# Kernel optimization log

Measured on AMD Instinct MI355X. Metric: run time of the kernel, lower is better.

Reference implementation:

```python
import jax, jax.numpy as jnp
import numpy as np

C, S, H = 64, 2048, 512
ITERATIONS = 3

def squash(x, eps=1e-07):
    # per-vector squash along last dim: (|x|^2/(1+|x|^2)) * x/|x|
    sq = jnp.sum(x * x, axis=-1, keepdims=True)
    safe_norm = jnp.sqrt(sq + eps)
    scale = sq / (1.0 + sq)
    return scale * (x / safe_norm)

def setup_inputs() -> dict:
    key = jax.random.key(0)
    k1, k2 = jax.random.split(key)
    x = jax.random.normal(k1, (C * S, H), dtype=jnp.float32)
    # xavier-normal init for Linear(H, H)
    std = np.sqrt(2.0 / (H + H)).astype(np.float32)
    W_weight = jax.random.normal(k2, (H, H), dtype=jnp.float32) * std
    W_bias = jnp.zeros((H,), dtype=jnp.float32)
    return {"x": x, "W_weight": W_weight, "W_bias": W_bias}

def reference(x, W_weight, W_bias):
    xr = x.reshape(C, S, H)
    # e_ij = squash(Linear(x))  -> [C, S, H]
    e_ij = squash(jnp.einsum('csh,oh->cso', xr, W_weight) + W_bias)
    b_ij = jnp.zeros((C, S), dtype=x.dtype)
    c_i = jnp.zeros((C, H), dtype=x.dtype)
    for _ in range(ITERATIONS):
        d_i = jax.nn.softmax(b_ij, axis=1)[..., None]          # [C, S, 1]
        c_i = squash(jnp.sum(d_i * e_ij, axis=1))              # [C, H]
        b_ij = b_ij + jnp.einsum('csh,ch->cs', e_ij, c_i)      # [C, S]
    return c_i
```

## Files before the change

### kernel.cpp

```cpp
#include <hip/hip_runtime.h>
#include <hip/hip_fp16.h>

#define HDIM 512

typedef __fp16 fp16x2 __attribute__((ext_vector_type(2)));
typedef _Float16 h8 __attribute__((ext_vector_type(8)));
typedef __attribute__((ext_vector_type(4))) float floatx4;

__device__ __forceinline__ void lds_barrier() {
  asm volatile("s_waitcnt lgkmcnt(0)\n\ts_barrier" ::: "memory");
}
__device__ __forceinline__ void issue_fence() {
  asm volatile("" ::: "memory");
}

__global__ __launch_bounds__(256) void prep_w_kernel(
    const float* __restrict__ W, _Float16* __restrict__ wf) {
  int i = (blockIdx.x * 256 + threadIdx.x) * 4;
  float4 f = *(const float4*)(W + i);
  wf[i + 0] = (_Float16)f.x;
  wf[i + 1] = (_Float16)f.y;
  wf[i + 2] = (_Float16)f.z;
  wf[i + 3] = (_Float16)f.w;
}

#define XS_H (128 * 40)
#define WS_H (512 * 32)

__device__ __forceinline__ void issue_w_dma(const _Float16* __restrict__ wf,
                                            _Float16* dst, int kt, int tid,
                                            int widx) {
#pragma unroll
  for (int q = 0; q < 4; ++q) {
    int idx = q * 512 + tid;
    int n = idx >> 2;
    int src = (idx & 3) ^ ((n >> 1) & 3);
    size_t goff = (size_t)n * HDIM + kt * 32 + src * 8;
    __builtin_amdgcn_global_load_lds(
        (const __attribute__((address_space(1))) void*)(wf + goff),
        (__attribute__((address_space(3))) void*)(dst +
                                                  (q * 512 + widx * 64) * 8),
        16, 0, 0);
  }
}

__global__ __launch_bounds__(512, 2) void gemm_kernel(
    const float* __restrict__ x, const _Float16* __restrict__ wf,
    const float* __restrict__ bias, __half* __restrict__ e,
    float* __restrict__ u_part, float* __restrict__ den_part) {
  __shared__ __align__(16) _Float16 smem[2 * XS_H + 3 * WS_H];
  _Float16* xs[2] = {smem, smem + XS_H};
  _Float16* wsm = smem + 2 * XS_H;

  const int tid = threadIdx.x;
  const int lane = tid & 63;
  const int widx = tid >> 6;
  const int wave_m = widx >> 2;
  const int wave_n = widx & 3;
  const int lrow = lane & 15, quad = lane >> 4;

  const int bid = blockIdx.x;
  const int row0 = bid * 128;

  const int xrow = tid >> 2;
  const int xcg = tid & 3;
  const float* xbase = x + (size_t)(row0 + xrow) * HDIM + xcg * 8;

  floatx4 acc[4][8];
#pragma unroll
  for (int i = 0; i < 4; ++i)
#pragma unroll
    for (int j = 0; j < 8; ++j) acc[i][j] = (floatx4){0.f, 0.f, 0.f, 0.f};

  float4 xr[2][2];

  issue_w_dma(wf, wsm + 0 * WS_H, 0, tid, widx);
  issue_fence();
  xr[0][0] = *(const float4*)xbase;
  xr[0][1] = *(const float4*)(xbase + 4);
  issue_fence();
  issue_w_dma(wf, wsm + 1 * WS_H, 1, tid, widx);
  issue_fence();
  xr[1][0] = *(const float4*)(xbase + 32);
  xr[1][1] = *(const float4*)(xbase + 36);
  issue_fence();

  const int chunkB = quad ^ ((lrow >> 1) & 3);

#pragma unroll
  for (int t = 0; t < 16; ++t) {
    {
      float4 a0 = xr[t & 1][0], a1 = xr[t & 1][1];
      union { h8 v8; fp16x2 v2[4]; } u;
      u.v2[0] = __builtin_amdgcn_cvt_pkrtz(a0.x, a0.y);
      u.v2[1] = __builtin_amdgcn_cvt_pkrtz(a0.z, a0.w);
      u.v2[2] = __builtin_amdgcn_cvt_pkrtz(a1.x, a1.y);
      u.v2[3] = __builtin_amdgcn_cvt_pkrtz(a1.z, a1.w);
      *(h8*)&xs[t & 1][xrow * 40 + xcg * 8] = u.v8;
    }
    lds_barrier();
    if (t <= 13) {
      issue_w_dma(wf, wsm + ((t + 2) % 3) * WS_H, t + 2, tid, widx);
      issue_fence();
      const float* gp = xbase + (t + 2) * 32;
      xr[t & 1][0] = *(const float4*)gp;
      xr[t & 1][1] = *(const float4*)(gp + 4);
      issue_fence();
    }
    const _Float16* xsr = xs[t & 1];
    const _Float16* wcur = wsm + (t % 3) * WS_H;
    h8 a[4], bh[8];
#pragma unroll
    for (int mt = 0; mt < 4; ++mt)
      a[mt] = *(const h8*)&xsr[(wave_m * 64 + mt * 16 + lrow) * 40 + quad * 8];
#pragma unroll
    for (int nt = 0; nt < 8; ++nt)
      bh[nt] =
          *(const h8*)&wcur[(wave_n * 128 + nt * 16 + lrow) * 32 + chunkB * 8];
    __builtin_amdgcn_s_setprio(1);
#pragma unroll
    for (int mt = 0; mt < 4; ++mt)
#pragma unroll
      for (int nt = 0; nt < 8; ++nt)
        acc[mt][nt] = __builtin_amdgcn_mfma_f32_16x16x32_f16(
            a[mt], bh[nt], acc[mt][nt], 0, 0, 0);
    __builtin_amdgcn_s_setprio(0);
  }

  float* sqp = (float*)smem;
  float* scs = (float*)smem + 512;
  float* upl = (float*)smem + 640;

  float bias_v[8];
  int colg[8];
#pragma unroll
  for (int nt = 0; nt < 8; ++nt) {
    colg[nt] = wave_n * 128 + nt * 16 + lrow;
    bias_v[nt] = bias[colg[nt]];
  }
#pragma unroll
  for (int mt = 0; mt < 4; ++mt) {
#pragma unroll
    for (int r = 0; r < 4; ++r) {
      float s = 0.f;
#pragma unroll
      for (int nt = 0; nt < 8; ++nt) {
        float yv = acc[mt][nt][r] + bias_v[nt];
        s += yv * yv;
      }
      s += __shfl_xor(s, 1, 64);
      s += __shfl_xor(s, 2, 64);
      s += __shfl_xor(s, 4, 64);
      s += __shfl_xor(s, 8, 64);
      if (lrow == 0)
        sqp[wave_n * 128 + wave_m * 64 + mt * 16 + quad * 4 + r] = s;
    }
  }
  lds_barrier();
  if (tid < 128) {
    float s = sqp[tid] + sqp[128 + tid] + sqp[256 + tid] + sqp[384 + tid];
    scs[tid] = s / ((1.f + s) * sqrtf(s + 1e-7f));
  }
  lds_barrier();

  float up[8] = {0.f, 0.f, 0.f, 0.f, 0.f, 0.f, 0.f, 0.f};
#pragma unroll
  for (int mt = 0; mt < 4; ++mt) {
#pragma unroll
    for (int r = 0; r < 4; ++r) {
      int row_local = wave_m * 64 + mt * 16 + quad * 4 + r;
      float scv = scs[row_local];
      __half* erow = e + (size_t)(row0 + row_local) * HDIM;
#pragma unroll
      for (int nt = 0; nt < 8; ++nt) {
        float ev = (acc[mt][nt][r] + bias_v[nt]) * scv;
        erow[colg[nt]] = __float2half(ev);
        up[nt] += ev;
      }
    }
  }
#pragma unroll
  for (int nt = 0; nt < 8; ++nt) {
    float v = up[nt];
    v += __shfl_xor(v, 16, 64);
    v += __shfl_xor(v, 32, 64);
    if (quad == 0) upl[wave_m * 512 + colg[nt]] = v;
  }
  lds_barrier();
  u_part[(size_t)bid * HDIM + tid] = upl[tid] + upl[512 + tid];
  if (tid == 0) den_part[bid] = 128.0f;
}

__global__ __launch_bounds__(256) void kbv_kernel(
    const __half* __restrict__ e, float* __restrict__ b,
    const float* __restrict__ c_buf, float* __restrict__ u_part,
    float* __restrict__ den_part) {
  const int w = threadIdx.x >> 6;
  const int lane = threadIdx.x & 63;
  const int wave_g = blockIdx.x * 4 + w;
  const int cap = wave_g >> 6;
  const int chunk = wave_g & 63;
  const int r0 = cap * 2048 + chunk * 32;

  float c8[8];
  {
    const float4* cp = (const float4*)(c_buf + cap * HDIM + lane * 8);
    float4 ca = cp[0], cb = cp[1];
    c8[0] = ca.x; c8[1] = ca.y; c8[2] = ca.z; c8[3] = ca.w;
    c8[4] = cb.x; c8[5] = cb.y; c8[6] = cb.z; c8[7] = cb.w;
  }
  float u8[8] = {0, 0, 0, 0, 0, 0, 0, 0};
  float den = 0.f;

  union U { int4 v; __half hh[8]; };
  U cur[4], nxt[4];
  const __half* yb = e + (size_t)r0 * HDIM + lane * 8;
#pragma unroll
  for (int j = 0; j < 4; ++j) cur[j].v = *(const int4*)(yb + (size_t)j * HDIM);

  for (int g = 0; g < 8; ++g) {
    const int rg = r0 + g * 4;
    if (g < 7) {
#pragma unroll
      for (int j = 0; j < 4; ++j)
        nxt[j].v = *(const int4*)(yb + (size_t)(g * 4 + 4 + j) * HDIM);
    }
    float bv[4];
#pragma unroll
    for (int j = 0; j < 4; ++j) bv[j] = b[rg + j];
    float dot[4];
#pragma unroll
    for (int j = 0; j < 4; ++j) {
      float d = 0.f;
#pragma unroll
      for (int k = 0; k < 8; ++k) d += __half2float(cur[j].hh[k]) * c8[k];
      dot[j] = d;
    }
#pragma unroll
    for (int s = 1; s < 64; s <<= 1) {
#pragma unroll
      for (int j = 0; j < 4; ++j) dot[j] += __shfl_xor(dot[j], s, 64);
    }
#pragma unroll
    for (int j = 0; j < 4; ++j) {
      float bn = bv[j] + dot[j];
      if (lane == 0) b[rg + j] = bn;
      float wj = __expf(bn);
      den += wj;
#pragma unroll
      for (int k = 0; k < 8; ++k) u8[k] += wj * __half2float(cur[j].hh[k]);
    }
#pragma unroll
    for (int j = 0; j < 4; ++j) cur[j] = nxt[j];
  }

  __shared__ float lred[4][512];
  __shared__ float ldn[4];
#pragma unroll
  for (int k = 0; k < 8; ++k) lred[w][lane * 8 + k] = u8[k];
  if (lane == 0) ldn[w] = den;
  __syncthreads();
  const int t = threadIdx.x;
  const int blkc = blockIdx.x & 15;
#pragma unroll
  for (int hh = 0; hh < 2; ++hh) {
    int h = hh * 256 + t;
    float v = lred[0][h] + lred[1][h] + lred[2][h] + lred[3][h];
    u_part[((size_t)cap * 16 + blkc) * HDIM + h] = v;
  }
  if (t == 0)
    den_part[cap * 16 + blkc] = ldn[0] + ldn[1] + ldn[2] + ldn[3];
}

__global__ __launch_bounds__(512) void kcsq_kernel(
    const float* __restrict__ u_part, const float* __restrict__ den_part,
    float* __restrict__ out) {
  const int cap = blockIdx.x;
  const int t = threadIdx.x;
  __shared__ float red[512];
  __shared__ float sden;

  if (t < 16) red[t] = den_part[cap * 16 + t];
  __syncthreads();
  if (t == 0) {
    float s = 0.f;
#pragma unroll
    for (int i = 0; i < 16; ++i) s += red[i];
    sden = s;
  }
  __syncthreads();
  const float den = sden;

  float v = 0.f;
  const float* up = u_part + (size_t)cap * 16 * HDIM + t;
#pragma unroll
  for (int ch = 0; ch < 16; ++ch) v += up[ch * HDIM];
  v /= den;

  red[t] = v * v;
  __syncthreads();
  for (int s = 256; s > 0; s >>= 1) {
    if (t < s) red[t] += red[t + s];
    __syncthreads();
  }
  const float sqv = red[0];
  const float scv = sqv / ((1.f + sqv) * sqrtf(sqv + 1e-7f));
  out[cap * HDIM + t] = v * scv;
}

extern "C" void kernel_launch(void* const* d_in, const int* in_sizes, int n_in,
                              void* d_out, int out_size, void* d_ws,
                              size_t ws_size, hipStream_t stream) {
  const float* x = (const float*)d_in[0];
  const float* W = (const float*)d_in[1];
  const float* bias = (const float*)d_in[2];
  float* out = (float*)d_out;
  char* ws = (char*)d_ws;

  __half* e = (__half*)ws;
  float* b = (float*)(ws + (size_t)134217728);
  float* c_buf = b + 131072;
  float* u_part = c_buf + 32768;
  float* den_part = u_part + (size_t)64 * 16 * 512;
  _Float16* wf = (_Float16*)(den_part + 1024);

  (void)hipMemsetAsync(b, 0, (size_t)131072 * sizeof(float), stream);

  prep_w_kernel<<<256, 256, 0, stream>>>(W, wf);
  gemm_kernel<<<1024, 512, 0, stream>>>(x, wf, bias, e, u_part, den_part);

  kcsq_kernel<<<64, 512, 0, stream>>>(u_part, den_part, c_buf);
  kbv_kernel<<<1024, 256, 0, stream>>>(e, b, c_buf, u_part, den_part);
  kcsq_kernel<<<64, 512, 0, stream>>>(u_part, den_part, c_buf);
  kbv_kernel<<<1024, 256, 0, stream>>>(e, b, c_buf, u_part, den_part);
  kcsq_kernel<<<64, 512, 0, stream>>>(u_part, den_part, out);
}
```

Baseline: 476.5 us.

## Deepen GEMM W-tile ring, move barrier after prefetch, and split kbv finer

The GEMM moves from a 3-deep to a 4-deep LDS ring for W tiles and issues the next DMA and x loads before the barrier. The W swizzle is adjusted to match. kbv now uses 16 rows per wave with a 3-stage register buffer and a single per-lane b load broadcast via shuffle, doubling the grid. kcsq takes a variable chunk count and gains an extra barrier before reusing its shared buffer. The larger LDS footprint may reduce GEMM blocks per CU.

```diff
diff --git a/kernel.cpp b/kernel.cpp
--- a/kernel.cpp
+++ b/kernel.cpp
@@ -34,7 +34,7 @@
   for (int q = 0; q < 4; ++q) {
     int idx = q * 512 + tid;
     int n = idx >> 2;
-    int src = (idx & 3) ^ ((n >> 1) & 3);
+    int src = (idx & 3) ^ ((n >> 2) & 3);
     size_t goff = (size_t)n * HDIM + kt * 32 + src * 8;
     __builtin_amdgcn_global_load_lds(
         (const __attribute__((address_space(1))) void*)(wf + goff),
@@ -48,7 +48,7 @@
     const float* __restrict__ x, const _Float16* __restrict__ wf,
     const float* __restrict__ bias, __half* __restrict__ e,
     float* __restrict__ u_part, float* __restrict__ den_part) {
-  __shared__ __align__(16) _Float16 smem[2 * XS_H + 3 * WS_H];
+  __shared__ __align__(16) _Float16 smem[2 * XS_H + 4 * WS_H];
   _Float16* xs[2] = {smem, smem + XS_H};
   _Float16* wsm = smem + 2 * XS_H;
 
@@ -85,7 +85,7 @@
   xr[1][1] = *(const float4*)(xbase + 36);
   issue_fence();
 
-  const int chunkB = quad ^ ((lrow >> 1) & 3);
+  const int chunkB = quad ^ ((lrow >> 2) & 3);
 
 #pragma unroll
   for (int t = 0; t < 16; ++t) {
@@ -98,17 +98,17 @@
       u.v2[3] = __builtin_amdgcn_cvt_pkrtz(a1.z, a1.w);
       *(h8*)&xs[t & 1][xrow * 40 + xcg * 8] = u.v8;
     }
-    lds_barrier();
     if (t <= 13) {
-      issue_w_dma(wf, wsm + ((t + 2) % 3) * WS_H, t + 2, tid, widx);
+      issue_w_dma(wf, wsm + ((t + 2) & 3) * WS_H, t + 2, tid, widx);
       issue_fence();
       const float* gp = xbase + (t + 2) * 32;
       xr[t & 1][0] = *(const float4*)gp;
       xr[t & 1][1] = *(const float4*)(gp + 4);
       issue_fence();
     }
+    lds_barrier();
     const _Float16* xsr = xs[t & 1];
-    const _Float16* wcur = wsm + (t % 3) * WS_H;
+    const _Float16* wcur = wsm + (t & 3) * WS_H;
     h8 a[4], bh[8];
 #pragma unroll
     for (int mt = 0; mt < 4; ++mt)
@@ -187,8 +187,9 @@
     if (quad == 0) upl[wave_m * 512 + colg[nt]] = v;
   }
   lds_barrier();
-  u_part[(size_t)bid * HDIM + tid] = upl[tid] + upl[512 + tid];
-  if (tid == 0) den_part[bid] = 128.0f;
+  u_part[(size_t)((bid >> 4) * 32 + (bid & 15)) * HDIM + tid] =
+      upl[tid] + upl[512 + tid];
+  if (tid == 0) den_part[(bid >> 4) * 32 + (bid & 15)] = 128.0f;
 }
 
 __global__ __launch_bounds__(256) void kbv_kernel(
@@ -198,9 +199,9 @@
   const int w = threadIdx.x >> 6;
   const int lane = threadIdx.x & 63;
   const int wave_g = blockIdx.x * 4 + w;
-  const int cap = wave_g >> 6;
-  const int chunk = wave_g & 63;
-  const int r0 = cap * 2048 + chunk * 32;
+  const int cap = wave_g >> 7;
+  const int chunk = wave_g & 127;
+  const int r0 = cap * 2048 + chunk * 16;
 
   float c8[8];
   {
@@ -209,25 +210,29 @@
     c8[0] = ca.x; c8[1] = ca.y; c8[2] = ca.z; c8[3] = ca.w;
     c8[4] = cb.x; c8[5] = cb.y; c8[6] = cb.z; c8[7] = cb.w;
   }
+  const float bline = b[r0 + (lane & 15)];
   float u8[8] = {0, 0, 0, 0, 0, 0, 0, 0};
   float den = 0.f;
 
   union U { int4 v; __half hh[8]; };
-  U cur[4], nxt[4];
+  U buf[3][4];
   const __half* yb = e + (size_t)r0 * HDIM + lane * 8;
 #pragma unroll
-  for (int j = 0; j < 4; ++j) cur[j].v = *(const int4*)(yb + (size_t)j * HDIM);
-
-  for (int g = 0; g < 8; ++g) {
+  for (int j = 0; j < 4; ++j) buf[0][j].v = *(const int4*)(yb + (size_t)j * HDIM);
+#pragma unroll
+  for (int j = 0; j < 4; ++j)
+    buf[1][j].v = *(const int4*)(yb + (size_t)(4 + j) * HDIM);
+
+#pragma unroll
+  for (int g = 0; g < 4; ++g) {
     const int rg = r0 + g * 4;
-    if (g < 7) {
+    if (g < 2) {
 #pragma unroll
       for (int j = 0; j < 4; ++j)
-        nxt[j].v = *(const int4*)(yb + (size_t)(g * 4 + 4 + j) * HDIM);
-    }
-    float bv[4];
-#pragma unroll
-    for (int j = 0; j < 4; ++j) bv[j] = b[rg + j];
+        buf[(g + 2) % 3][j].v =
+            *(const int4*)(yb + (size_t)((g + 2) * 4 + j) * HDIM);
+    }
+    const U* cur = buf[g % 3];
     float dot[4];
 #pragma unroll
     for (int j = 0; j < 4; ++j) {
@@ -243,15 +248,13 @@
     }
 #pragma unroll
     for (int j = 0; j < 4; ++j) {
-      float bn = bv[j] + dot[j];
+      float bn = __shfl(bline, g * 4 + j, 64) + dot[j];
       if (lane == 0) b[rg + j] = bn;
       float wj = __expf(bn);
       den += wj;
 #pragma unroll
       for (int k = 0; k < 8; ++k) u8[k] += wj * __half2float(cur[j].hh[k]);
     }
-#pragma unroll
-    for (int j = 0; j < 4; ++j) cur[j] = nxt[j];
   }
 
   __shared__ float lred[4][512];
@@ -261,42 +264,41 @@
   if (lane == 0) ldn[w] = den;
   __syncthreads();
   const int t = threadIdx.x;
-  const int blkc = blockIdx.x & 15;
+  const int blkc = blockIdx.x & 31;
 #pragma unroll
   for (int hh = 0; hh < 2; ++hh) {
     int h = hh * 256 + t;
     float v = lred[0][h] + lred[1][h] + lred[2][h] + lred[3][h];
-    u_part[((size_t)cap * 16 + blkc) * HDIM + h] = v;
+    u_part[((size_t)cap * 32 + blkc) * HDIM + h] = v;
   }
   if (t == 0)
-    den_part[cap * 16 + blkc] = ldn[0] + ldn[1] + ldn[2] + ldn[3];
+    den_part[cap * 32 + blkc] = ldn[0] + ldn[1] + ldn[2] + ldn[3];
 }
 
 __global__ __launch_bounds__(512) void kcsq_kernel(
     const float* __restrict__ u_part, const float* __restrict__ den_part,
-    float* __restrict__ out) {
+    float* __restrict__ out, int nch) {
   const int cap = blockIdx.x;
   const int t = threadIdx.x;
   __shared__ float red[512];
   __shared__ float sden;
 
-  if (t < 16) red[t] = den_part[cap * 16 + t];
+  if (t < nch) red[t] = den_part[cap * 32 + t];
   __syncthreads();
   if (t == 0) {
     float s = 0.f;
-#pragma unroll
-    for (int i = 0; i < 16; ++i) s += red[i];
+    for (int i = 0; i < nch; ++i) s += red[i];
     sden = s;
   }
   __syncthreads();
   const float den = sden;
 
   float v = 0.f;
-  const float* up = u_part + (size_t)cap * 16 * HDIM + t;
-#pragma unroll
-  for (int ch = 0; ch < 16; ++ch) v += up[ch * HDIM];
+  const float* up = u_part + (size_t)cap * 32 * HDIM + t;
+  for (int ch = 0; ch < nch; ++ch) v += up[ch * HDIM];
   v /= den;
 
+  __syncthreads();
   red[t] = v * v;
   __syncthreads();
   for (int s = 256; s > 0; s >>= 1) {
@@ -321,17 +323,17 @@
   float* b = (float*)(ws + (size_t)134217728);
   float* c_buf = b + 131072;
   float* u_part = c_buf + 32768;
-  float* den_part = u_part + (size_t)64 * 16 * 512;
-  _Float16* wf = (_Float16*)(den_part + 1024);
+  float* den_part = u_part + (size_t)64 * 32 * 512;
+  _Float16* wf = (_Float16*)(den_part + 2048);
 
   (void)hipMemsetAsync(b, 0, (size_t)131072 * sizeof(float), stream);
 
   prep_w_kernel<<<256, 256, 0, stream>>>(W, wf);
   gemm_kernel<<<1024, 512, 0, stream>>>(x, wf, bias, e, u_part, den_part);
 
-  kcsq_kernel<<<64, 512, 0, stream>>>(u_part, den_part, c_buf);
-  kbv_kernel<<<1024, 256, 0, stream>>>(e, b, c_buf, u_part, den_part);
-  kcsq_kernel<<<64, 512, 0, stream>>>(u_part, den_part, c_buf);
-  kbv_kernel<<<1024, 256, 0, stream>>>(e, b, c_buf, u_part, den_part);
-  kcsq_kernel<<<64, 512, 0, stream>>>(u_part, den_part, out);
-}
+  kcsq_kernel<<<64, 512, 0, stream>>>(u_part, den_part, c_buf, 16);
+  kbv_kernel<<<2048, 256, 0, stream>>>(e, b, c_buf, u_part, den_part);
+  kcsq_kernel<<<64, 512, 0, stream>>>(u_part, den_part, c_buf, 32);
+  kbv_kernel<<<2048, 256, 0, stream>>>(e, b, c_buf, u_part, den_part);
+  kcsq_kernel<<<64, 512, 0, stream>>>(u_part, den_part, out, 32);
+}
```

Result: slower. 498.0 us (+4.5%).

## Fuse squash into routing kernels and deepen GEMM W buffering to four stages

Applied to the files above, without the earlier changes.

Removes the two intermediate kcsq launches. Each routing block now recomputes the squashed capsule vector from the partial sums in its own prologue, and the first iteration uses a constant denominator and skips the memset of b. Ping-pong partial buffers avoid read/write races once the reduction moves inside the consumer kernel. In the GEMM, the W LDS ring grows from 3 to 4 slots and the barrier moves after the next DMA/x-load issue, so loads start earlier. In exchange, each of the 1024 blocks redundantly re-reduces 16x512 partials, and the larger shared memory footprint could reduce occupancy.

```diff
diff --git a/kernel.cpp b/kernel.cpp
--- a/kernel.cpp
+++ b/kernel.cpp
@@ -47,8 +47,8 @@
 __global__ __launch_bounds__(512, 2) void gemm_kernel(
     const float* __restrict__ x, const _Float16* __restrict__ wf,
     const float* __restrict__ bias, __half* __restrict__ e,
-    float* __restrict__ u_part, float* __restrict__ den_part) {
-  __shared__ __align__(16) _Float16 smem[2 * XS_H + 3 * WS_H];
+    float* __restrict__ u_gemm) {
+  __shared__ __align__(16) _Float16 smem[2 * XS_H + 4 * WS_H];
   _Float16* xs[2] = {smem, smem + XS_H};
   _Float16* wsm = smem + 2 * XS_H;
 
@@ -98,17 +98,17 @@
       u.v2[3] = __builtin_amdgcn_cvt_pkrtz(a1.z, a1.w);
       *(h8*)&xs[t & 1][xrow * 40 + xcg * 8] = u.v8;
     }
-    lds_barrier();
     if (t <= 13) {
-      issue_w_dma(wf, wsm + ((t + 2) % 3) * WS_H, t + 2, tid, widx);
+      issue_w_dma(wf, wsm + ((t + 2) & 3) * WS_H, t + 2, tid, widx);
       issue_fence();
       const float* gp = xbase + (t + 2) * 32;
       xr[t & 1][0] = *(const float4*)gp;
       xr[t & 1][1] = *(const float4*)(gp + 4);
       issue_fence();
     }
+    lds_barrier();
     const _Float16* xsr = xs[t & 1];
-    const _Float16* wcur = wsm + (t % 3) * WS_H;
+    const _Float16* wcur = wsm + (t & 3) * WS_H;
     h8 a[4], bh[8];
 #pragma unroll
     for (int mt = 0; mt < 4; ++mt)
@@ -187,47 +187,85 @@
     if (quad == 0) upl[wave_m * 512 + colg[nt]] = v;
   }
   lds_barrier();
-  u_part[(size_t)bid * HDIM + tid] = upl[tid] + upl[512 + tid];
-  if (tid == 0) den_part[bid] = 128.0f;
-}
-
-__global__ __launch_bounds__(256) void kbv_kernel(
-    const __half* __restrict__ e, float* __restrict__ b,
-    const float* __restrict__ c_buf, float* __restrict__ u_part,
-    float* __restrict__ den_part) {
-  const int w = threadIdx.x >> 6;
-  const int lane = threadIdx.x & 63;
-  const int wave_g = blockIdx.x * 4 + w;
-  const int cap = wave_g >> 6;
-  const int chunk = wave_g & 63;
-  const int r0 = cap * 2048 + chunk * 32;
+  u_gemm[(size_t)(bid >> 4) * 16 * HDIM + (size_t)(bid & 15) * HDIM + tid] =
+      upl[tid] + upl[512 + tid];
+}
+
+template <bool FIRST>
+__global__ __launch_bounds__(256, 4) void route_iter_kernel(
+    const __half* __restrict__ e, const float* __restrict__ u_in,
+    const float* __restrict__ den_in, float* __restrict__ b,
+    float* __restrict__ u_out, float* __restrict__ den_out) {
+  const int tid = threadIdx.x;
+  const int w = tid >> 6;
+  const int lane = tid & 63;
+  const int bid = blockIdx.x;
+  const int cap = bid >> 4;
+  const int r0 = bid * 128;
+
+  __shared__ float csh[512];
+  __shared__ float red[256];
+  __shared__ float lred[4][512];
+  __shared__ float ldn[4];
+  __shared__ float sden;
+
+  float v0 = 0.f, v1 = 0.f;
+  {
+    const float* upb = u_in + (size_t)cap * 16 * HDIM;
+#pragma unroll
+    for (int ch = 0; ch < 16; ++ch) {
+      v0 += upb[ch * HDIM + tid];
+      v1 += upb[ch * HDIM + tid + 256];
+    }
+  }
+  float den;
+  if (FIRST) {
+    den = 2048.f;
+  } else {
+    red[tid] = (tid < 16) ? den_in[cap * 16 + tid] : 0.f;
+    __syncthreads();
+    if (tid == 0) {
+      float s = 0.f;
+#pragma unroll
+      for (int i = 0; i < 16; ++i) s += red[i];
+      sden = s;
+    }
+    __syncthreads();
+    den = sden;
+    __syncthreads();
+  }
+  v0 /= den;
+  v1 /= den;
+  red[tid] = v0 * v0 + v1 * v1;
+  __syncthreads();
+  for (int s = 128; s > 0; s >>= 1) {
+    if (tid < s) red[tid] += red[tid + s];
+    __syncthreads();
+  }
+  const float sqv = red[0];
+  const float scv = sqv / ((1.f + sqv) * sqrtf(sqv + 1e-7f));
+  csh[tid] = v0 * scv;
+  csh[tid + 256] = v1 * scv;
+  __syncthreads();
 
   float c8[8];
-  {
-    const float4* cp = (const float4*)(c_buf + cap * HDIM + lane * 8);
-    float4 ca = cp[0], cb = cp[1];
-    c8[0] = ca.x; c8[1] = ca.y; c8[2] = ca.z; c8[3] = ca.w;
-    c8[4] = cb.x; c8[5] = cb.y; c8[6] = cb.z; c8[7] = cb.w;
-  }
+#pragma unroll
+  for (int k = 0; k < 8; ++k) c8[k] = csh[lane * 8 + k];
   float u8[8] = {0, 0, 0, 0, 0, 0, 0, 0};
-  float den = 0.f;
+  float den_w = 0.f;
 
   union U { int4 v; __half hh[8]; };
   U cur[4], nxt[4];
-  const __half* yb = e + (size_t)r0 * HDIM + lane * 8;
+  const __half* yb = e + (size_t)(r0 + w * 32) * HDIM + lane * 8;
 #pragma unroll
   for (int j = 0; j < 4; ++j) cur[j].v = *(const int4*)(yb + (size_t)j * HDIM);
 
   for (int g = 0; g < 8; ++g) {
-    const int rg = r0 + g * 4;
     if (g < 7) {
 #pragma unroll
       for (int j = 0; j < 4; ++j)
         nxt[j].v = *(const int4*)(yb + (size_t)(g * 4 + 4 + j) * HDIM);
     }
-    float bv[4];
-#pragma unroll
-    for (int j = 0; j < 4; ++j) bv[j] = b[rg + j];
     float dot[4];
 #pragma unroll
     for (int j = 0; j < 4; ++j) {
@@ -243,10 +281,11 @@
     }
 #pragma unroll
     for (int j = 0; j < 4; ++j) {
-      float bn = bv[j] + dot[j];
-      if (lane == 0) b[rg + j] = bn;
+      const int rl = w * 32 + g * 4 + j;
+      float bn = FIRST ? dot[j] : (b[r0 + rl] + dot[j]);
+      if (FIRST && lane == 0) b[r0 + rl] = bn;
       float wj = __expf(bn);
-      den += wj;
+      den_w += wj;
 #pragma unroll
       for (int k = 0; k < 8; ++k) u8[k] += wj * __half2float(cur[j].hh[k]);
     }
@@ -254,33 +293,29 @@
     for (int j = 0; j < 4; ++j) cur[j] = nxt[j];
   }
 
-  __shared__ float lred[4][512];
-  __shared__ float ldn[4];
 #pragma unroll
   for (int k = 0; k < 8; ++k) lred[w][lane * 8 + k] = u8[k];
-  if (lane == 0) ldn[w] = den;
-  __syncthreads();
-  const int t = threadIdx.x;
-  const int blkc = blockIdx.x & 15;
+  if (lane == 0) ldn[w] = den_w;
+  __syncthreads();
+  float* ur = u_out + (size_t)cap * 16 * HDIM + (size_t)(bid & 15) * HDIM;
 #pragma unroll
   for (int hh = 0; hh < 2; ++hh) {
-    int h = hh * 256 + t;
-    float v = lred[0][h] + lred[1][h] + lred[2][h] + lred[3][h];
-    u_part[((size_t)cap * 16 + blkc) * HDIM + h] = v;
-  }
-  if (t == 0)
-    den_part[cap * 16 + blkc] = ldn[0] + ldn[1] + ldn[2] + ldn[3];
-}
-
-__global__ __launch_bounds__(512) void kcsq_kernel(
-    const float* __restrict__ u_part, const float* __restrict__ den_part,
+    int h = hh * 256 + tid;
+    ur[h] = lred[0][h] + lred[1][h] + lred[2][h] + lred[3][h];
+  }
+  if (tid == 0)
+    den_out[cap * 16 + (bid & 15)] = ldn[0] + ldn[1] + ldn[2] + ldn[3];
+}
+
+__global__ __launch_bounds__(512) void route_final_kernel(
+    const float* __restrict__ u_in, const float* __restrict__ den_in,
     float* __restrict__ out) {
   const int cap = blockIdx.x;
   const int t = threadIdx.x;
   __shared__ float red[512];
   __shared__ float sden;
 
-  if (t < 16) red[t] = den_part[cap * 16 + t];
+  red[t] = (t < 16) ? den_in[cap * 16 + t] : 0.f;
   __syncthreads();
   if (t == 0) {
     float s = 0.f;
@@ -292,11 +327,12 @@
   const float den = sden;
 
   float v = 0.f;
-  const float* up = u_part + (size_t)cap * 16 * HDIM + t;
+  const float* up = u_in + (size_t)cap * 16 * HDIM + t;
 #pragma unroll
   for (int ch = 0; ch < 16; ++ch) v += up[ch * HDIM];
   v /= den;
 
+  __syncthreads();
   red[t] = v * v;
   __syncthreads();
   for (int s = 256; s > 0; s >>= 1) {
@@ -318,20 +354,20 @@
   char* ws = (char*)d_ws;
 
   __half* e = (__half*)ws;
-  float* b = (float*)(ws + (size_t)134217728);
-  float* c_buf = b + 131072;
-  float* u_part = c_buf + 32768;
-  float* den_part = u_part + (size_t)64 * 16 * 512;
-  _Float16* wf = (_Float16*)(den_part + 1024);
-
-  (void)hipMemsetAsync(b, 0, (size_t)131072 * sizeof(float), stream);
+  float* u_gemm = (float*)(ws + (size_t)134217728);
+  float* u_a = u_gemm + (size_t)64 * 16 * 512;
+  float* u_b = u_a + (size_t)64 * 16 * 512;
+  float* den_a = u_b + (size_t)64 * 16 * 512;
+  float* den_b = den_a + 1024;
+  float* b = den_b + 1024;
+  _Float16* wf = (_Float16*)(b + 131072);
 
   prep_w_kernel<<<256, 256, 0, stream>>>(W, wf);
-  gemm_kernel<<<1024, 512, 0, stream>>>(x, wf, bias, e, u_part, den_part);
-
-  kcsq_kernel<<<64, 512, 0, stream>>>(u_part, den_part, c_buf);
-  kbv_kernel<<<1024, 256, 0, stream>>>(e, b, c_buf, u_part, den_part);
-  kcsq_kernel<<<64, 512, 0, stream>>>(u_part, den_part, c_buf);
-  kbv_kernel<<<1024, 256, 0, stream>>>(e, b, c_buf, u_part, den_part);
-  kcsq_kernel<<<64, 512, 0, stream>>>(u_part, den_part, out);
-}
+  gemm_kernel<<<1024, 512, 0, stream>>>(x, wf, bias, e, u_gemm);
+
+  route_iter_kernel<true><<<1024, 256, 0, stream>>>(e, u_gemm, nullptr, b,
+                                                    u_a, den_a);
+  route_iter_kernel<false><<<1024, 256, 0, stream>>>(e, u_a, den_a, b,
+                                                     u_b, den_b);
+  route_final_kernel<<<64, 512, 0, stream>>>(u_b, den_b, out);
+}
```

After: 469.9 us. No clear change (-1.4%).
